# Kernel optimization log

Measured on AMD Instinct MI355X. Metric: run time of the kernel, lower is better.

Reference implementation:

```python
import jax, jax.numpy as jnp
import numpy as np

B, T, D, H = 64, 512, 512, 768
FORGET_BIAS = 1.0  # TF BasicLSTMCell default


def setup_inputs() -> dict:
    key = jax.random.key(0)
    k1, k2, k3, k4 = jax.random.split(key, 4)
    seq = jax.random.normal(k1, (B, T, D), dtype=jnp.float32)
    seq_len = jax.random.randint(k2, (B,), 1, T + 1).astype(jnp.int32)
    s = 1.0 / np.sqrt(D + H)
    W_fw = jax.random.uniform(k3, (D + H, 4 * H), jnp.float32, -s, s)
    W_bw = jax.random.uniform(k4, (D + H, 4 * H), jnp.float32, -s, s)
    b_fw = jnp.zeros((4 * H,), jnp.float32)
    b_bw = jnp.zeros((4 * H,), jnp.float32)
    return {"seq": seq, "seq_len": seq_len, "W_fw": W_fw, "b_fw": b_fw,
            "W_bw": W_bw, "b_bw": b_bw}


def _reverse_sequence(x, seq_len):
    # Mirrors tf.reverse_sequence along time axis 1.
    t = jnp.arange(x.shape[1])
    idx = jnp.where(t[None, :] < seq_len[:, None],
                    seq_len[:, None] - 1 - t[None, :], t[None, :])
    return jnp.take_along_axis(x, idx[:, :, None], axis=1)


def _lstm(x, seq_len, W, b):
    # x: [B, T, D]; W: [D+H, 4H] with TF gate order i, j, f, o.
    b_, t_, _ = x.shape
    h_dim = W.shape[1] // 4

    def step(carry, inp):
        c, h = carry
        x_t, t = inp
        gates = jnp.concatenate([x_t, h], axis=-1) @ W + b
        i, j, f, o = jnp.split(gates, 4, axis=-1)
        new_c = c * jax.nn.sigmoid(f + FORGET_BIAS) + jax.nn.sigmoid(i) * jnp.tanh(j)
        new_h = jnp.tanh(new_c) * jax.nn.sigmoid(o)
        mask = (t < seq_len)[:, None]
        c2 = jnp.where(mask, new_c, c)   # state copied through past seq_len
        h2 = jnp.where(mask, new_h, h)
        out = jnp.where(mask, new_h, jnp.zeros_like(new_h))  # dynamic_rnn zeros outputs
        return (c2, h2), out

    init = (jnp.zeros((b_, h_dim), x.dtype), jnp.zeros((b_, h_dim), x.dtype))
    xs = (jnp.swapaxes(x, 0, 1), jnp.arange(t_))
    (c, h), outs = jax.lax.scan(step, init, xs)
    return jnp.swapaxes(outs, 0, 1), h  # [B,T,H], [B,H]


def reference(seq, seq_len, W_fw, b_fw, W_bw, b_bw):
    out_fw, h_fw = _lstm(seq, seq_len, W_fw, b_fw)
    seq_rev = _reverse_sequence(seq, seq_len)
    out_bw_rev, h_bw = _lstm(seq_rev, seq_len, W_bw, b_bw)
    out_bw = _reverse_sequence(out_bw_rev, seq_len)
    outputs = jnp.concatenate([out_fw, out_bw], axis=-1)   # [B,T,2H]
    state_h = jnp.concatenate([h_fw, h_bw], axis=-1)       # [B,2H]
    return outputs, state_h
```

## Files before the change

### kernel.cpp

```cpp
#include <hip/hip_runtime.h>

#define NB 64
#define NT 512
#define ND 512
#define NH 768
#define KTOT 1280
#define NG 3072
#define NROW (NB * NT)
#define NHG 48
#define NCG 192
#define NKS 40

typedef short bf16x8 __attribute__((ext_vector_type(8)));
typedef float f32x4 __attribute__((ext_vector_type(4)));
typedef _Float16 f16x4 __attribute__((ext_vector_type(4)));

__device__ __forceinline__ unsigned short f2b(float f) {
    unsigned int u; __builtin_memcpy(&u, &f, 4);
    u = u + 0x7FFFu + ((u >> 16) & 1u);
    return (unsigned short)(u >> 16);
}
__device__ __forceinline__ float sigmoidf_(float x) { return 1.f / (1.f + __expf(-x)); }
__device__ __forceinline__ float tanhf_(float x) { return 2.f / (1.f + __expf(-2.f * x)) - 1.f; }

__global__ __launch_bounds__(256) void transpose_w(const float* __restrict__ W,
                                                   unsigned short* __restrict__ WTf) {
    __shared__ float tile[64][65];
    int bx = blockIdx.x % (NG / 64);
    int by = blockIdx.x / (NG / 64);
    int cb = bx * 64, kb = by * 64;
    int tid = threadIdx.x;
    {
        int r = tid >> 2;
        int coff = (tid & 3) * 16;
        const float* src = W + (size_t)(kb + r) * NG + cb + coff;
#pragma unroll
        for (int i = 0; i < 16; i += 4) {
            float4 v = *(const float4*)(src + i);
            tile[coff + i][r] = v.x; tile[coff + i + 1][r] = v.y;
            tile[coff + i + 2][r] = v.z; tile[coff + i + 3][r] = v.w;
        }
    }
    __syncthreads();
#pragma unroll
    for (int it = 0; it < 2; ++it) {
        int id = tid + it * 256;
        int ch = id >> 6;
        int l = id & 63;
        int cgi = ch & 3, ksi = ch >> 2;
        int c = cgi * 16 + (l & 15);
        int k = ksi * 32 + ((l >> 4) * 8);
        bf16x8 o;
#pragma unroll
        for (int j = 0; j < 8; ++j) o[j] = (short)f2b(tile[c][k + j]);
        size_t cg = (size_t)(cb / 16) + cgi;
        size_t ks = (size_t)(kb / 32) + ksi;
        *(bf16x8*)(WTf + ((cg * NKS + ks) * 64 + l) * 8) = o;
    }
}

__global__ __launch_bounds__(256) void convert_x(const float* __restrict__ src,
                                                 unsigned short* __restrict__ dst, int n8) {
    int i = blockIdx.x * 256 + threadIdx.x;
    if (i < n8) {
        const float4* s = (const float4*)(src + (size_t)i * 8);
        float4 v0 = s[0], v1 = s[1];
        bf16x8 o;
        o[0] = (short)f2b(v0.x); o[1] = (short)f2b(v0.y);
        o[2] = (short)f2b(v0.z); o[3] = (short)f2b(v0.w);
        o[4] = (short)f2b(v1.x); o[5] = (short)f2b(v1.y);
        o[6] = (short)f2b(v1.z); o[7] = (short)f2b(v1.w);
        *(bf16x8*)(dst + (size_t)i * 8) = o;
    }
}

__global__ __launch_bounds__(256) void gemm_xw(
    const float* __restrict__ seq,
    const unsigned short* __restrict__ WTf,
    const float* __restrict__ b_fw,
    const float* __restrict__ b_bw,
    _Float16* __restrict__ Gx) {
    __shared__ unsigned short Albs[64 * 522];
    int blk = blockIdx.x;
    int dir = blk >> 9;
    int mbi = blk & 511;
    int mb = mbi * 64;
    const float* bias = dir ? b_bw : b_fw;
    int tid = threadIdx.x;
    {
        int r = tid >> 2;
        int c = tid & 3;
        const float* src = seq + (size_t)(mb + r) * ND;
#pragma unroll
        for (int i = 0; i < 16; ++i) {
            int k = c * 8 + i * 32;
            float4 v0 = *(const float4*)(src + k);
            float4 v1 = *(const float4*)(src + k + 4);
            bf16x8 o;
            o[0] = (short)f2b(v0.x); o[1] = (short)f2b(v0.y);
            o[2] = (short)f2b(v0.z); o[3] = (short)f2b(v0.w);
            o[4] = (short)f2b(v1.x); o[5] = (short)f2b(v1.y);
            o[6] = (short)f2b(v1.z); o[7] = (short)f2b(v1.w);
            *(bf16x8*)&Albs[r * 522 + k] = o;
        }
    }
    __syncthreads();
    int lane = tid & 63, wave = tid >> 6;
    int r0 = lane & 15, qq = lane >> 4, q8 = qq * 8;
    _Float16* gbase = Gx + (size_t)(dir * 512 + mbi) * 196608;
#pragma unroll 1
    for (int nc = 0; nc < 12; ++nc) {
        int colbase = wave * NH + nc * 64;
        f32x4 acc[4][4];
#pragma unroll
        for (int nt = 0; nt < 4; ++nt) {
            float bv = bias[colbase + nt * 16 + r0] + (wave == 2 ? 1.0f : 0.0f);
#pragma unroll
            for (int m = 0; m < 4; ++m) {
                acc[m][nt][0] = bv; acc[m][nt][1] = bv;
                acc[m][nt][2] = bv; acc[m][nt][3] = bv;
            }
        }
        const unsigned short* fpre = WTf +
            ((size_t)(dir * NCG + wave * NHG + nc * 4) * NKS) * 512 + (size_t)lane * 8;
#pragma unroll
        for (int ks = 0; ks < 16; ++ks) {
            bf16x8 a[4], bb[4];
#pragma unroll
            for (int m = 0; m < 4; ++m)
                a[m] = *(const bf16x8*)&Albs[(m * 16 + r0) * 522 + ks * 32 + q8];
#pragma unroll
            for (int nt = 0; nt < 4; ++nt)
                bb[nt] = *(const bf16x8*)(fpre + ((size_t)nt * NKS + ks) * 512);
#pragma unroll
            for (int m = 0; m < 4; ++m)
#pragma unroll
                for (int nt = 0; nt < 4; ++nt)
                    acc[m][nt] = __builtin_amdgcn_mfma_f32_16x16x32_bf16(a[m], bb[nt], acc[m][nt], 0, 0, 0);
        }
#pragma unroll
        for (int nt = 0; nt < 4; ++nt) {
#pragma unroll
            for (int m = 0; m < 4; ++m) {
                f16x4 o;
                o[0] = (_Float16)acc[m][nt][0]; o[1] = (_Float16)acc[m][nt][1];
                o[2] = (_Float16)acc[m][nt][2]; o[3] = (_Float16)acc[m][nt][3];
                *(f16x4*)(gbase + (size_t)((((nc * 4 + wave) * 4 + nt) * 4 + m) * 64 + lane) * 4) = o;
            }
        }
    }
}

__global__ __launch_bounds__(256, 1) void lstm_persistent(
    const float* __restrict__ seq,
    const unsigned short* __restrict__ xbf,
    int mode,
    const int* __restrict__ seq_len,
    const unsigned short* __restrict__ WTf,
    const float* __restrict__ bias_fw,
    const float* __restrict__ bias_bw,
    const _Float16* __restrict__ Gx,
    unsigned short* __restrict__ hbufs,
    float* __restrict__ h_final,
    float* __restrict__ out,
    unsigned int* __restrict__ barrier_cnts)
{
    extern __shared__ char smem[];
    unsigned short* Whf = (unsigned short*)smem;
    unsigned short* Af  = (unsigned short*)(smem + 98304);
    float* gl = (float*)(smem + 147456);

    int bid = blockIdx.x;
    int hgroup = bid % NHG;
    int bgroup = (bid / NHG) & 1;
    int dir = bid / (2 * NHG);
    int grp = bid / NHG;
    int b0 = bgroup * 32;
    int hbase = hgroup * 16;
    int tid = threadIdx.x;
    int lane = tid & 63;
    int wave = tid >> 6;
    int r0 = lane & 15;
    int qq = lane >> 4;
    int q8 = qq * 8;

    const float* bias = dir ? bias_bw : bias_fw;
    int col = wave * NH + hbase + r0;
    float bv = bias[col] + (wave == 2 ? 1.0f : 0.0f);

    {
#pragma unroll
        for (int i = 0; i < 24; ++i) {
            int g = i / 6;
            int ks = wave + (i % 6) * 4;
            const unsigned short* src = WTf +
                ((size_t)(dir * NCG + g * NHG + hgroup) * NKS + 16 + ks) * 512 + (size_t)lane * 8;
            *(bf16x8*)(Whf + ((size_t)tid + (size_t)i * 256) * 8) = *(const bf16x8*)src;
        }
    }

    int ebl0 = tid >> 4;
    int ehl = tid & 15;
    int hidx = hbase + ehl;
    int Lb[2]; Lb[0] = seq_len[b0 + ebl0]; Lb[1] = seq_len[b0 + ebl0 + 16];
    float c_reg[2] = {0.f, 0.f};
    unsigned short h_reg[2] = {0, 0};

    f32x4 ax0, ax1;
    float gxv[8];
    int Rlo[8], Roff[8];
    const _Float16* GxK;
    int Lx[2];

    if (mode == 2) {
        size_t K0 = (size_t)dir * 100663296 + (size_t)(hgroup >> 2) * 16384 +
                    (size_t)wave * 4096 + (size_t)(hgroup & 3) * 1024 + (size_t)r0 * 4;
        GxK = Gx + K0;
#pragma unroll
        for (int i = 0; i < 8; ++i) {
            int br = b0 + (i >> 2) * 16 + qq * 4 + (i & 3);
            int L = seq_len[br];
            Rlo[i] = br * NT;
            Roff[i] = dir ? (L - 1) : 0;
        }
    } else {
        Lx[0] = seq_len[b0 + r0];
        Lx[1] = seq_len[b0 + 16 + r0];
    }

    auto gxload = [&](int stepn) {
#pragma unroll
        for (int i = 0; i < 8; ++i) {
            int tn = dir ? (Roff[i] - stepn) : stepn;
            tn = tn < 0 ? 0 : (tn > NT - 1 ? NT - 1 : tn);
            int R = Rlo[i] + tn;
            size_t a = (size_t)(R >> 6) * 196608 +
                       (size_t)(((R >> 4) & 3) * 256 + ((R >> 2) & 3) * 64 + (R & 3));
            gxv[i] = (float)GxK[a];
        }
    };

    const unsigned short* fbx = WTf +
        ((size_t)(dir * NCG + wave * NHG + hgroup) * NKS) * 512 + (size_t)lane * 8;

    auto xwindow = [&](int stepn) {
#pragma unroll
        for (int i = 0; i < 8; ++i) {
            int m = i >> 2;
            int ks = wave + (i & 3) * 4;
            int row = b0 + m * 16 + r0;
            int tn = dir ? (Lx[m] - 1 - stepn) : stepn;
            tn = tn < 0 ? 0 : (tn > NT - 1 ? NT - 1 : tn);
            unsigned short* dst = Af + ((size_t)(m * 24 + ks) * 64 + lane) * 8;
            if (mode == 1) {
                *(bf16x8*)dst = *(const bf16x8*)(xbf + ((size_t)row * NT + tn) * ND + ks * 32 + q8);
            } else {
                const float* xr = seq + ((size_t)row * NT + tn) * ND + ks * 32 + q8;
                float4 v0 = *(const float4*)xr, v1 = *(const float4*)(xr + 4);
                bf16x8 o;
                o[0] = (short)f2b(v0.x); o[1] = (short)f2b(v0.y);
                o[2] = (short)f2b(v0.z); o[3] = (short)f2b(v0.w);
                o[4] = (short)f2b(v1.x); o[5] = (short)f2b(v1.y);
                o[6] = (short)f2b(v1.z); o[7] = (short)f2b(v1.w);
                *(bf16x8*)dst = o;
            }
        }
        __syncthreads();
        ax0[0] = bv; ax0[1] = bv; ax0[2] = bv; ax0[3] = bv;
        ax1 = ax0;
        const unsigned short* afp = Af + (size_t)lane * 8;
#pragma unroll
        for (int ks = 0; ks < 16; ++ks) {
            bf16x8 a0 = *(const bf16x8*)(afp + ks * 512);
            bf16x8 a1 = *(const bf16x8*)(afp + 12288 + ks * 512);
            bf16x8 bx = *(const bf16x8*)(fbx + (size_t)ks * 512);
            ax0 = __builtin_amdgcn_mfma_f32_16x16x32_bf16(a0, bx, ax0, 0, 0, 0);
            ax1 = __builtin_amdgcn_mfma_f32_16x16x32_bf16(a1, bx, ax1, 0, 0, 0);
        }
    };

    if (mode == 2) gxload(0); else xwindow(0);
    __syncthreads();

    unsigned int* cnt = barrier_cnts + grp * 64;

    for (int step = 0; step < NT; ++step) {
        const unsigned short* hin = hbufs + (size_t)(step % 3) * (2 * NB * NH) + (size_t)dir * NB * NH;
        unsigned short* hout      = hbufs + (size_t)((step + 1) % 3) * (2 * NB * NH) + (size_t)dir * NB * NH;

        {
            const unsigned long long* hb =
                (const unsigned long long*)(hin + (size_t)(b0 + r0) * NH + q8);
            unsigned long long hA[24];
#pragma unroll
            for (int i = 0; i < 12; ++i) {
                int off8 = ((i / 6) * 16 * NH + (wave + (i % 6) * 4) * 32) >> 2;
                hA[2 * i]     = __hip_atomic_load(hb + off8,     __ATOMIC_RELAXED, __HIP_MEMORY_SCOPE_AGENT);
                hA[2 * i + 1] = __hip_atomic_load(hb + off8 + 1, __ATOMIC_RELAXED, __HIP_MEMORY_SCOPE_AGENT);
            }
#pragma unroll
            for (int i = 0; i < 12; ++i) {
                union { unsigned long long u[2]; bf16x8 v; } t;
                t.u[0] = hA[2 * i]; t.u[1] = hA[2 * i + 1];
                *(bf16x8*)(Af + ((size_t)tid + (size_t)i * 256) * 8) = t.v;
            }
        }
        __syncthreads();

        f32x4 acc0, acc1;
        if (mode == 2) {
            acc0[0] = gxv[0]; acc0[1] = gxv[1]; acc0[2] = gxv[2]; acc0[3] = gxv[3];
            acc1[0] = gxv[4]; acc1[1] = gxv[5]; acc1[2] = gxv[6]; acc1[3] = gxv[7];
        } else {
            acc0 = ax0; acc1 = ax1;
        }
        {
            const unsigned short* afp = Af + (size_t)lane * 8;
            const unsigned short* wfp = Whf + (size_t)wave * 12288 + (size_t)lane * 8;
#pragma unroll
            for (int ks = 0; ks < 24; ++ks) {
                bf16x8 a0 = *(const bf16x8*)(afp + ks * 512);
                bf16x8 a1 = *(const bf16x8*)(afp + 12288 + ks * 512);
                bf16x8 wb = *(const bf16x8*)(wfp + ks * 512);
                acc0 = __builtin_amdgcn_mfma_f32_16x16x32_bf16(a0, wb, acc0, 0, 0, 0);
                acc1 = __builtin_amdgcn_mfma_f32_16x16x32_bf16(a1, wb, acc1, 0, 0, 0);
            }
        }

#pragma unroll
        for (int r = 0; r < 4; ++r) {
            gl[(wave * 32 + qq * 4 + r) * 17 + r0] = acc0[r];
            gl[(wave * 32 + 16 + qq * 4 + r) * 17 + r0] = acc1[r];
        }
        __syncthreads();

#pragma unroll
        for (int it = 0; it < 2; ++it) {
            int bl = ebl0 + it * 16;
            int bb = b0 + bl;
            if (step < Lb[it]) {
                float gi = gl[(0 * 32 + bl) * 17 + ehl];
                float gj = gl[(1 * 32 + bl) * 17 + ehl];
                float gf = gl[(2 * 32 + bl) * 17 + ehl];
                float go = gl[(3 * 32 + bl) * 17 + ehl];
                float nc = c_reg[it] * sigmoidf_(gf) + sigmoidf_(gi) * tanhf_(gj);
                float nh = tanhf_(nc) * sigmoidf_(go);
                c_reg[it] = nc;
                h_reg[it] = f2b(nh);
                if (step == Lb[it] - 1)
                    h_final[((size_t)dir * NB + bb) * NH + hidx] = nh;
                int t_out = dir ? (Lb[it] - 1 - step) : step;
                out[((size_t)bb * NT + t_out) * (2 * NH) + dir * NH + hidx] = nh;
            } else {
                out[((size_t)bb * NT + step) * (2 * NH) + dir * NH + hidx] = 0.f;
            }
            __hip_atomic_store(&hout[(size_t)bb * NH + hidx], h_reg[it],
                               __ATOMIC_RELAXED, __HIP_MEMORY_SCOPE_AGENT);
        }

        __syncthreads();

        if (tid == 0)
            __hip_atomic_fetch_add(cnt, 1u, __ATOMIC_RELEASE, __HIP_MEMORY_SCOPE_WORKGROUP);

        if (mode == 2) gxload(step + 1); else xwindow(step + 1);

        if (tid == 0) {
            unsigned int tgt = 48u * (unsigned)(step + 1);
            while (__hip_atomic_load(cnt, __ATOMIC_RELAXED, __HIP_MEMORY_SCOPE_AGENT) < tgt)
                __builtin_amdgcn_s_sleep(2);
        }
        __syncthreads();
    }
}

__global__ __launch_bounds__(256) void write_state(const float* __restrict__ h_final,
                                                   float* __restrict__ out_state) {
    int i = blockIdx.x * 256 + threadIdx.x;
    if (i < 2 * NB * NH) {
        int dir = i / (NB * NH);
        int rem = i - dir * (NB * NH);
        int b = rem / NH, h = rem - (rem / NH) * NH;
        out_state[(size_t)b * (2 * NH) + dir * NH + h] = h_final[i];
    }
}

extern "C" void kernel_launch(void* const* d_in, const int* in_sizes, int n_in,
                              void* d_out, int out_size, void* d_ws, size_t ws_size,
                              hipStream_t stream) {
    const float* seq   = (const float*)d_in[0];
    const int* seq_len = (const int*)d_in[1];
    const float* W_fw  = (const float*)d_in[2];
    const float* b_fw  = (const float*)d_in[3];
    const float* W_bw  = (const float*)d_in[4];
    const float* b_bw  = (const float*)d_in[5];
    float* out = (float*)d_out;

    char* ws = (char*)d_ws;
    size_t off = 0;
    unsigned short* WTf = (unsigned short*)(ws + off); off += (size_t)2 * NG * KTOT * 2;
    unsigned short* hbufs = (unsigned short*)(ws + off);
    size_t hbuf_bytes = (size_t)3 * 2 * NB * NH * 2;   off += hbuf_bytes;
    float* h_final = (float*)(ws + off);
    size_t hf_bytes = (size_t)2 * NB * NH * 4;         off += hf_bytes;
    unsigned int* barrier_cnts = (unsigned int*)(ws + off);
    size_t bar_bytes = 1024;                           off += bar_bytes;

    _Float16* Gx = (_Float16*)(ws + off);
    size_t gx_bytes = (size_t)2 * 512 * 196608 * 2;
    unsigned short* xbf = (unsigned short*)(ws + off);
    size_t xbf_bytes = (size_t)NB * NT * ND * 2;

    int mode = (ws_size >= off + gx_bytes) ? 2
             : ((ws_size >= off + xbf_bytes) ? 1 : 0);

    hipMemsetAsync(hbufs, 0, hbuf_bytes + hf_bytes + bar_bytes, stream);

    transpose_w<<<(KTOT / 64) * (NG / 64), 256, 0, stream>>>(W_fw, WTf);
    transpose_w<<<(KTOT / 64) * (NG / 64), 256, 0, stream>>>(W_bw, WTf + (size_t)NG * KTOT);

    if (mode == 2) {
        gemm_xw<<<1024, 256, 0, stream>>>(seq, WTf, b_fw, b_bw, Gx);
    } else if (mode == 1) {
        int n8 = NB * NT * ND / 8;
        convert_x<<<(n8 + 255) / 256, 256, 0, stream>>>(seq, xbf, n8);
    }

    size_t smem_bytes = 156160;
    lstm_persistent<<<192, 256, smem_bytes, stream>>>(
        seq, xbf, mode, seq_len, WTf, b_fw, b_bw, Gx,
        hbufs, h_final, out, barrier_cnts);

    write_state<<<(2 * NB * NH + 255) / 256, 256, 0, stream>>>(
        h_final, out + (size_t)NB * NT * 2 * NH);
}
```

Measured before the change: 3.513 ms.

## Store h in MFMA fragment layout and stream it directly into registers

The hidden state is now written to global memory in a pre-swizzled MFMA A-fragment layout, so each wave loads its fragments directly into registers with pipelined chunked loads. This replaces the LDS staging step and its barrier. The recurrent weight slice is also hoisted into registers once, before the time loop, and the x-window path loads fragments straight from global memory. Together these cut the per-step LDS traffic and one __syncthreads, at the cost of higher register pressure (24 weight vectors plus 48 in-flight loads) and a smaller LDS allocation.

```diff
diff --git a/kernel.cpp b/kernel.cpp
--- a/kernel.cpp
+++ b/kernel.cpp
@@ -167,8 +167,7 @@
 {
     extern __shared__ char smem[];
     unsigned short* Whf = (unsigned short*)smem;
-    unsigned short* Af  = (unsigned short*)(smem + 98304);
-    float* gl = (float*)(smem + 147456);
+    float* gl = (float*)(smem + 98304);
 
     int bid = blockIdx.x;
     int hgroup = bid % NHG;
@@ -205,6 +204,13 @@
     int Lb[2]; Lb[0] = seq_len[b0 + ebl0]; Lb[1] = seq_len[b0 + ebl0 + 16];
     float c_reg[2] = {0.f, 0.f};
     unsigned short h_reg[2] = {0, 0};
+    size_t eoff[2];
+#pragma unroll
+    for (int it = 0; it < 2; ++it) {
+        int bb = b0 + ebl0 + it * 16;
+        eoff[it] = ((size_t)((bb >> 4) * 24 + (hidx >> 5)) * 64 +
+                    (size_t)(((hidx >> 3) & 3) * 16 + (bb & 15))) * 8 + (hidx & 7);
+    }
 
     f32x4 ax0, ax1;
     float gxv[8];
@@ -244,68 +250,64 @@
         ((size_t)(dir * NCG + wave * NHG + hgroup) * NKS) * 512 + (size_t)lane * 8;
 
     auto xwindow = [&](int stepn) {
-#pragma unroll
-        for (int i = 0; i < 8; ++i) {
-            int m = i >> 2;
-            int ks = wave + (i & 3) * 4;
+        ax0[0] = bv; ax0[1] = bv; ax0[2] = bv; ax0[3] = bv;
+        ax1 = ax0;
+#pragma unroll
+        for (int m = 0; m < 2; ++m) {
             int row = b0 + m * 16 + r0;
             int tn = dir ? (Lx[m] - 1 - stepn) : stepn;
             tn = tn < 0 ? 0 : (tn > NT - 1 ? NT - 1 : tn);
-            unsigned short* dst = Af + ((size_t)(m * 24 + ks) * 64 + lane) * 8;
-            if (mode == 1) {
-                *(bf16x8*)dst = *(const bf16x8*)(xbf + ((size_t)row * NT + tn) * ND + ks * 32 + q8);
-            } else {
-                const float* xr = seq + ((size_t)row * NT + tn) * ND + ks * 32 + q8;
-                float4 v0 = *(const float4*)xr, v1 = *(const float4*)(xr + 4);
-                bf16x8 o;
-                o[0] = (short)f2b(v0.x); o[1] = (short)f2b(v0.y);
-                o[2] = (short)f2b(v0.z); o[3] = (short)f2b(v0.w);
-                o[4] = (short)f2b(v1.x); o[5] = (short)f2b(v1.y);
-                o[6] = (short)f2b(v1.z); o[7] = (short)f2b(v1.w);
-                *(bf16x8*)dst = o;
-            }
-        }
-        __syncthreads();
-        ax0[0] = bv; ax0[1] = bv; ax0[2] = bv; ax0[3] = bv;
-        ax1 = ax0;
-        const unsigned short* afp = Af + (size_t)lane * 8;
-#pragma unroll
-        for (int ks = 0; ks < 16; ++ks) {
-            bf16x8 a0 = *(const bf16x8*)(afp + ks * 512);
-            bf16x8 a1 = *(const bf16x8*)(afp + 12288 + ks * 512);
-            bf16x8 bx = *(const bf16x8*)(fbx + (size_t)ks * 512);
-            ax0 = __builtin_amdgcn_mfma_f32_16x16x32_bf16(a0, bx, ax0, 0, 0, 0);
-            ax1 = __builtin_amdgcn_mfma_f32_16x16x32_bf16(a1, bx, ax1, 0, 0, 0);
+#pragma unroll
+            for (int ks = 0; ks < 16; ++ks) {
+                bf16x8 av;
+                if (mode == 1) {
+                    av = *(const bf16x8*)(xbf + ((size_t)row * NT + tn) * ND + ks * 32 + q8);
+                } else {
+                    const float* xr = seq + ((size_t)row * NT + tn) * ND + ks * 32 + q8;
+                    float4 v0 = *(const float4*)xr, v1 = *(const float4*)(xr + 4);
+                    av[0] = (short)f2b(v0.x); av[1] = (short)f2b(v0.y);
+                    av[2] = (short)f2b(v0.z); av[3] = (short)f2b(v0.w);
+                    av[4] = (short)f2b(v1.x); av[5] = (short)f2b(v1.y);
+                    av[6] = (short)f2b(v1.z); av[7] = (short)f2b(v1.w);
+                }
+                bf16x8 bx = *(const bf16x8*)(fbx + (size_t)ks * 512);
+                if (m == 0) ax0 = __builtin_amdgcn_mfma_f32_16x16x32_bf16(av, bx, ax0, 0, 0, 0);
+                else        ax1 = __builtin_amdgcn_mfma_f32_16x16x32_bf16(av, bx, ax1, 0, 0, 0);
+            }
         }
     };
 
     if (mode == 2) gxload(0); else xwindow(0);
     __syncthreads();
 
+    bf16x8 wb[24];
+    {
+        const unsigned short* wfp = Whf + (size_t)wave * 12288 + (size_t)lane * 8;
+#pragma unroll
+        for (int ks = 0; ks < 24; ++ks) wb[ks] = *(const bf16x8*)(wfp + ks * 512);
+    }
+
     unsigned int* cnt = barrier_cnts + grp * 64;
+    int rb0 = bgroup * 2;
 
     for (int step = 0; step < NT; ++step) {
-        const unsigned short* hin = hbufs + (size_t)(step % 3) * (2 * NB * NH) + (size_t)dir * NB * NH;
-        unsigned short* hout      = hbufs + (size_t)((step + 1) % 3) * (2 * NB * NH) + (size_t)dir * NB * NH;
-
-        {
-            const unsigned long long* hb =
-                (const unsigned long long*)(hin + (size_t)(b0 + r0) * NH + q8);
-            unsigned long long hA[24];
-#pragma unroll
-            for (int i = 0; i < 12; ++i) {
-                int off8 = ((i / 6) * 16 * NH + (wave + (i % 6) * 4) * 32) >> 2;
-                hA[2 * i]     = __hip_atomic_load(hb + off8,     __ATOMIC_RELAXED, __HIP_MEMORY_SCOPE_AGENT);
-                hA[2 * i + 1] = __hip_atomic_load(hb + off8 + 1, __ATOMIC_RELAXED, __HIP_MEMORY_SCOPE_AGENT);
-            }
-#pragma unroll
-            for (int i = 0; i < 12; ++i) {
-                union { unsigned long long u[2]; bf16x8 v; } t;
-                t.u[0] = hA[2 * i]; t.u[1] = hA[2 * i + 1];
-                *(bf16x8*)(Af + ((size_t)tid + (size_t)i * 256) * 8) = t.v;
-            }
-        }
-        __syncthreads();
+        const unsigned long long* hin64 = (const unsigned long long*)
+            (hbufs + (size_t)(step % 3) * (2 * NB * NH) + (size_t)dir * NB * NH);
+        unsigned short* hout = hbufs + (size_t)((step + 1) % 3) * (2 * NB * NH) + (size_t)dir * NB * NH;
+
+        unsigned long long huA[24], huB[24];
+        auto issue = [&](int c, unsigned long long* hu) {
+#pragma unroll
+            for (int i = 0; i < 6; ++i) {
+                int ks = c * 6 + i;
+                size_t o0 = ((size_t)(rb0 * 24 + ks) * 64 + lane) * 2;
+                size_t o1 = ((size_t)((rb0 + 1) * 24 + ks) * 64 + lane) * 2;
+                hu[4 * i]     = __hip_atomic_load(hin64 + o0,     __ATOMIC_RELAXED, __HIP_MEMORY_SCOPE_AGENT);
+                hu[4 * i + 1] = __hip_atomic_load(hin64 + o0 + 1, __ATOMIC_RELAXED, __HIP_MEMORY_SCOPE_AGENT);
+                hu[4 * i + 2] = __hip_atomic_load(hin64 + o1,     __ATOMIC_RELAXED, __HIP_MEMORY_SCOPE_AGENT);
+                hu[4 * i + 3] = __hip_atomic_load(hin64 + o1 + 1, __ATOMIC_RELAXED, __HIP_MEMORY_SCOPE_AGENT);
+            }
+        };
 
         f32x4 acc0, acc1;
         if (mode == 2) {
@@ -314,18 +316,25 @@
         } else {
             acc0 = ax0; acc1 = ax1;
         }
-        {
-            const unsigned short* afp = Af + (size_t)lane * 8;
-            const unsigned short* wfp = Whf + (size_t)wave * 12288 + (size_t)lane * 8;
-#pragma unroll
-            for (int ks = 0; ks < 24; ++ks) {
-                bf16x8 a0 = *(const bf16x8*)(afp + ks * 512);
-                bf16x8 a1 = *(const bf16x8*)(afp + 12288 + ks * 512);
-                bf16x8 wb = *(const bf16x8*)(wfp + ks * 512);
-                acc0 = __builtin_amdgcn_mfma_f32_16x16x32_bf16(a0, wb, acc0, 0, 0, 0);
-                acc1 = __builtin_amdgcn_mfma_f32_16x16x32_bf16(a1, wb, acc1, 0, 0, 0);
-            }
-        }
+
+        auto consume = [&](int c, const unsigned long long* hu) {
+#pragma unroll
+            for (int i = 0; i < 6; ++i) {
+                int ks = c * 6 + i;
+                union { unsigned long long u[2]; bf16x8 v; } fa0, fa1;
+                fa0.u[0] = hu[4 * i];     fa0.u[1] = hu[4 * i + 1];
+                fa1.u[0] = hu[4 * i + 2]; fa1.u[1] = hu[4 * i + 3];
+                acc0 = __builtin_amdgcn_mfma_f32_16x16x32_bf16(fa0.v, wb[ks], acc0, 0, 0, 0);
+                acc1 = __builtin_amdgcn_mfma_f32_16x16x32_bf16(fa1.v, wb[ks], acc1, 0, 0, 0);
+            }
+        };
+
+        issue(0, huA);
+        issue(1, huB);
+        consume(0, huA); issue(2, huA);
+        consume(1, huB); issue(3, huB);
+        consume(2, huA);
+        consume(3, huB);
 
 #pragma unroll
         for (int r = 0; r < 4; ++r) {
@@ -354,7 +363,7 @@
             } else {
                 out[((size_t)bb * NT + step) * (2 * NH) + dir * NH + hidx] = 0.f;
             }
-            __hip_atomic_store(&hout[(size_t)bb * NH + hidx], h_reg[it],
+            __hip_atomic_store(&hout[eoff[it]], h_reg[it],
                                __ATOMIC_RELAXED, __HIP_MEMORY_SCOPE_AGENT);
         }
 
@@ -426,7 +435,7 @@
         convert_x<<<(n8 + 255) / 256, 256, 0, stream>>>(seq, xbf, n8);
     }
 
-    size_t smem_bytes = 156160;
+    size_t smem_bytes = 98304 + 8704;
     lstm_persistent<<<192, 256, smem_bytes, stream>>>(
         seq, xbf, mode, seq_len, WTf, b_fw, b_bw, Gx,
         hbufs, h_final, out, barrier_cnts);
```

New measurement: 4.063 ms. 15.6% more time.
